# Kernel optimization log

Hardware: AMD Instinct MI355X
Metric: run time of the kernel (lower is better)

Reference implementation:

```python
import jax, jax.numpy as jnp
import numpy as np

B, H, S, DK = 2, 8, 4096, 64


def setup_inputs() -> dict:
    key = jax.random.key(0)
    kq, kk, kv = jax.random.split(key, 3)
    Q = jax.random.normal(kq, (B, H, S, DK), dtype=jnp.float32)
    K = jax.random.normal(kk, (B, H, S, DK), dtype=jnp.float32)
    V = jax.random.normal(kv, (B, H, S, DK), dtype=jnp.float32)
    attn_mask = jnp.zeros((1,), dtype=bool)  # accepted but unused by the module
    return {"Q": Q, "K": K, "V": V, "attn_mask": attn_mask}


def reference(Q, K, V, attn_mask):
    d_k = Q.shape[-1]
    scale = 1.0 / np.sqrt(d_k).astype(np.float32)
    # scores: [b, h, q, k] -- full O(n^2) matrix, as in the original
    scores = jnp.einsum('bhqd,bhkd->bhqk', Q, K) * scale
    attn = jax.nn.softmax(scores, axis=-1)
    context = jnp.einsum('bhqk,bhkd->bhqd', attn, V)
    return (context, attn)
```

## Files before the change

### kernel.cpp

```cpp
#include <hip/hip_runtime.h>
#include <hip/hip_bf16.h>


typedef __bf16 bf16x8 __attribute__((ext_vector_type(8)));
typedef __bf16 bf16x4 __attribute__((ext_vector_type(4)));
typedef float f32x4 __attribute__((ext_vector_type(4)));

#define BH 16
#define SEQ 4096
#define DKD 64
#define PSTRIDE 72
#define LOG2E 1.44269504088896f

__global__ void cvt_bf16_kernel(const float* __restrict__ src,
                                __bf16* __restrict__ dst, int n4, float scale) {
    int i = blockIdx.x * blockDim.x + threadIdx.x;
    if (i < n4) {
        const float4 v = reinterpret_cast<const float4*>(src)[i];
        bf16x4 o;
        o[0] = (__bf16)(v.x * scale); o[1] = (__bf16)(v.y * scale);
        o[2] = (__bf16)(v.z * scale); o[3] = (__bf16)(v.w * scale);
        reinterpret_cast<bf16x4*>(dst)[i] = o;
    }
}

__global__ void transpose_v_kernel(const float* __restrict__ V,
                                   __bf16* __restrict__ Vt) {
    __shared__ __bf16 T[DKD][72];
    const int head = blockIdx.y;
    const int s0 = blockIdx.x * 64;
    const int t = threadIdx.x;
    const float* vp = V + ((size_t)head * SEQ + s0) * DKD;
#pragma unroll
    for (int i = 0; i < 16; ++i) {
        int j = i * 256 + t;
        T[j & 63][j >> 6] = (__bf16)vp[j];
    }
    __syncthreads();
    __bf16* op = Vt + (size_t)head * DKD * SEQ + s0;
#pragma unroll
    for (int i = 0; i < 16; ++i) {
        int j = i * 256 + t;
        op[(size_t)(j >> 6) * SEQ + (j & 63)] = T[j >> 6][j & 63];
    }
}

__global__ __launch_bounds__(256, 4) void attn_kernel(
    const __bf16* __restrict__ Qb, const __bf16* __restrict__ Kb,
    const __bf16* __restrict__ Vt, float* __restrict__ out_ctx,
    float* __restrict__ out_attn) {
    __shared__ __align__(16) __bf16 Pl[2][4][16][PSTRIDE];
    __shared__ float Lsum[4][16];

    const int tid = threadIdx.x;
    const int w = tid >> 6;
    const int lane = tid & 63;
    const int c16 = lane & 15;
    const int g = lane >> 4;
    const int qsub = w & 1;
    const int khalf = w >> 1;

    const int wg = blockIdx.x;
    const int head = ((wg & 7) << 1) | ((wg >> 3) & 1);
    const int qblk = wg >> 4;
    const int qbase = qblk * 32 + qsub * 16;
    const int tile0 = khalf * 32;

    const __bf16* qp = Qb + ((size_t)head * SEQ + qbase + c16) * DKD + g * 8;
    const bf16x8 qf0 = *reinterpret_cast<const bf16x8*>(qp);
    const bf16x8 qf1 = *reinterpret_cast<const bf16x8*>(qp + 32);

    const __bf16* kbase = Kb + (size_t)head * SEQ * DKD;
    const __bf16* vbase = Vt + (size_t)head * DKD * SEQ;
    float* attn_p = out_attn + ((size_t)head * SEQ + qbase) * SEQ;

    float lsum = 0.f;
    for (int t = 0; t < 32; ++t) {
        const int kt = (tile0 + t) * 64;
#pragma unroll
        for (int ct = 0; ct < 4; ++ct) {
            const __bf16* kp = kbase + (size_t)(kt + ct * 16 + c16) * DKD + g * 8;
            bf16x8 kf0 = *reinterpret_cast<const bf16x8*>(kp);
            bf16x8 kf1 = *reinterpret_cast<const bf16x8*>(kp + 32);
            f32x4 a = (f32x4){0.f, 0.f, 0.f, 0.f};
            a = __builtin_amdgcn_mfma_f32_16x16x32_bf16(kf0, qf0, a, 0, 0, 0);
            a = __builtin_amdgcn_mfma_f32_16x16x32_bf16(kf1, qf1, a, 0, 0, 0);
            float e0 = __builtin_amdgcn_exp2f(a[0] * LOG2E);
            float e1 = __builtin_amdgcn_exp2f(a[1] * LOG2E);
            float e2 = __builtin_amdgcn_exp2f(a[2] * LOG2E);
            float e3 = __builtin_amdgcn_exp2f(a[3] * LOG2E);
            lsum += (e0 + e1) + (e2 + e3);
        }
    }
    lsum += __shfl_xor(lsum, 16);
    lsum += __shfl_xor(lsum, 32);
    if (g == 0) Lsum[w][c16] = lsum;
    __syncthreads();
    const float inv_l = __builtin_amdgcn_rcpf(Lsum[w][c16] + Lsum[w ^ 2][c16]);

    f32x4 o[4];
#pragma unroll
    for (int dt = 0; dt < 4; ++dt) o[dt] = (f32x4){0.f, 0.f, 0.f, 0.f};

    auto computeS = [&](int t, __bf16(*Pbuf)[PSTRIDE]) {
        const int kt = (tile0 + t) * 64;
        f32x4 acc[4];
#pragma unroll
        for (int ct = 0; ct < 4; ++ct) {
            acc[ct] = (f32x4){0.f, 0.f, 0.f, 0.f};
            const __bf16* kp = kbase + (size_t)(kt + ct * 16 + c16) * DKD + g * 8;
            bf16x8 kf0 = *reinterpret_cast<const bf16x8*>(kp);
            bf16x8 kf1 = *reinterpret_cast<const bf16x8*>(kp + 32);
            acc[ct] = __builtin_amdgcn_mfma_f32_16x16x32_bf16(kf0, qf0, acc[ct], 0, 0, 0);
            acc[ct] = __builtin_amdgcn_mfma_f32_16x16x32_bf16(kf1, qf1, acc[ct], 0, 0, 0);
        }
#pragma unroll
        for (int ct = 0; ct < 4; ++ct) {
            bf16x4 pb;
#pragma unroll
            for (int r = 0; r < 4; ++r)
                pb[r] = (__bf16)(__builtin_amdgcn_exp2f(acc[ct][r] * LOG2E) * inv_l);
            *reinterpret_cast<bf16x4*>(&Pbuf[c16][ct * 16 + g * 4]) = pb;
        }
    };

    auto pvTile = [&](int t, const __bf16(*Pbuf)[PSTRIDE]) {
        const int kt = (tile0 + t) * 64;
        bf16x8 pb0 = *reinterpret_cast<const bf16x8*>(&Pbuf[c16][g * 8]);
        bf16x8 pb1 = *reinterpret_cast<const bf16x8*>(&Pbuf[c16][g * 8 + 32]);
#pragma unroll
        for (int dt = 0; dt < 4; ++dt) {
            const __bf16* vp = vbase + (size_t)(dt * 16 + c16) * SEQ + kt + g * 8;
            bf16x8 vf0 = *reinterpret_cast<const bf16x8*>(vp);
            bf16x8 vf1 = *reinterpret_cast<const bf16x8*>(vp + 32);
            o[dt] = __builtin_amdgcn_mfma_f32_16x16x32_bf16(vf0, pb0, o[dt], 0, 0, 0);
            o[dt] = __builtin_amdgcn_mfma_f32_16x16x32_bf16(vf1, pb1, o[dt], 0, 0, 0);
        }
    };

    auto storeAttn = [&](int t, const __bf16(*Pbuf)[PSTRIDE]) {
        const int kt = (tile0 + t) * 64;
#pragma unroll
        for (int r4 = 0; r4 < 4; ++r4) {
            const int row = r4 * 4 + g;
            bf16x4 pb = *reinterpret_cast<const bf16x4*>(&Pbuf[row][c16 * 4]);
            f32x4 v;
#pragma unroll
            for (int j = 0; j < 4; ++j) v[j] = (float)pb[j];
            *reinterpret_cast<f32x4*>(attn_p + (size_t)row * SEQ + kt + c16 * 4) = v;
        }
    };

    computeS(0, Pl[0][w]);
    for (int t = 1; t < 31; t += 2) {
        computeS(t, Pl[1][w]);
        pvTile(t - 1, Pl[0][w]);
        storeAttn(t - 1, Pl[0][w]);
        computeS(t + 1, Pl[0][w]);
        pvTile(t, Pl[1][w]);
        storeAttn(t, Pl[1][w]);
    }
    computeS(31, Pl[1][w]);
    pvTile(30, Pl[0][w]);
    storeAttn(30, Pl[0][w]);
    pvTile(31, Pl[1][w]);
    storeAttn(31, Pl[1][w]);

    __syncthreads();
    float* Of = reinterpret_cast<float*>(&Pl[0][0][0][0]);
    float* my = Of + ((size_t)qsub * 16 + c16) * 64;
    if (khalf == 1) {
#pragma unroll
        for (int dt = 0; dt < 4; ++dt)
            *reinterpret_cast<f32x4*>(my + dt * 16 + g * 4) = o[dt];
    }
    __syncthreads();
    if (khalf == 0) {
        float* ctx_p = out_ctx + ((size_t)head * SEQ + qbase) * DKD;
#pragma unroll
        for (int dt = 0; dt < 4; ++dt) {
            f32x4 p = *reinterpret_cast<const f32x4*>(my + dt * 16 + g * 4);
            o[dt] += p;
            *reinterpret_cast<f32x4*>(ctx_p + (size_t)c16 * DKD + dt * 16 + g * 4) = o[dt];
        }
    }
}

extern "C" void kernel_launch(void* const* d_in, const int* in_sizes, int n_in,
                              void* d_out, int out_size, void* d_ws, size_t ws_size,
                              hipStream_t stream) {
    const float* Q = (const float*)d_in[0];
    const float* K = (const float*)d_in[1];
    const float* V = (const float*)d_in[2];
    float* out = (float*)d_out;

    const size_t nElem = (size_t)BH * SEQ * DKD;
    __bf16* Qb = (__bf16*)d_ws;
    __bf16* Kb = Qb + nElem;
    __bf16* Vt = Kb + nElem;

    float* out_ctx = out;
    float* out_attn = out + nElem;

    const int n4 = (int)(nElem / 4);
    cvt_bf16_kernel<<<dim3((n4 + 255) / 256), dim3(256), 0, stream>>>(Q, Qb, n4, 0.125f);
    cvt_bf16_kernel<<<dim3((n4 + 255) / 256), dim3(256), 0, stream>>>(K, Kb, n4, 1.0f);
    transpose_v_kernel<<<dim3(64, BH), dim3(256), 0, stream>>>(V, Vt);
    attn_kernel<<<dim3(BH * SEQ / 32), dim3(256), 0, stream>>>(Qb, Kb, Vt, out_ctx, out_attn);
}
```

Baseline: 765.4 us.

## Split row-sum pass into its own kernel and store fp32 attn directly from registers

The softmax denominator pass moves into a separate lsum kernel that writes the row sums to workspace, and the main kernel reads them back. This frees the attention kernel from the shared-memory sum buffer and its block barrier. The attention probabilities are now written in fp32 straight from the MFMA accumulators instead of being reread from bf16 shared memory. That gives full fp32 precision in attn and removes an LDS round trip. The trade-off is an extra kernel launch and strided 16-byte stores per row, which may coalesce worse than the previous row-contiguous stores.

```diff
diff --git a/kernel.cpp b/kernel.cpp
--- a/kernel.cpp
+++ b/kernel.cpp
@@ -45,11 +45,9 @@
     }
 }
 
-__global__ __launch_bounds__(256, 4) void attn_kernel(
+__global__ __launch_bounds__(256, 4) void lsum_kernel(
     const __bf16* __restrict__ Qb, const __bf16* __restrict__ Kb,
-    const __bf16* __restrict__ Vt, float* __restrict__ out_ctx,
-    float* __restrict__ out_attn) {
-    __shared__ __align__(16) __bf16 Pl[2][4][16][PSTRIDE];
+    float* __restrict__ Lsum_ws) {
     __shared__ float Lsum[4][16];
 
     const int tid = threadIdx.x;
@@ -69,10 +67,7 @@
     const __bf16* qp = Qb + ((size_t)head * SEQ + qbase + c16) * DKD + g * 8;
     const bf16x8 qf0 = *reinterpret_cast<const bf16x8*>(qp);
     const bf16x8 qf1 = *reinterpret_cast<const bf16x8*>(qp + 32);
-
     const __bf16* kbase = Kb + (size_t)head * SEQ * DKD;
-    const __bf16* vbase = Vt + (size_t)head * DKD * SEQ;
-    float* attn_p = out_attn + ((size_t)head * SEQ + qbase) * SEQ;
 
     float lsum = 0.f;
     for (int t = 0; t < 32; ++t) {
@@ -96,7 +91,39 @@
     lsum += __shfl_xor(lsum, 32);
     if (g == 0) Lsum[w][c16] = lsum;
     __syncthreads();
-    const float inv_l = __builtin_amdgcn_rcpf(Lsum[w][c16] + Lsum[w ^ 2][c16]);
+    if (khalf == 0 && g == 0)
+        Lsum_ws[(size_t)head * SEQ + qbase + c16] = Lsum[w][c16] + Lsum[w ^ 2][c16];
+}
+
+__global__ __launch_bounds__(256, 4) void attn_kernel(
+    const __bf16* __restrict__ Qb, const __bf16* __restrict__ Kb,
+    const __bf16* __restrict__ Vt, const float* __restrict__ Lsum_ws,
+    float* __restrict__ out_ctx, float* __restrict__ out_attn) {
+    __shared__ __align__(16) __bf16 Pl[2][4][16][PSTRIDE];
+
+    const int tid = threadIdx.x;
+    const int w = tid >> 6;
+    const int lane = tid & 63;
+    const int c16 = lane & 15;
+    const int g = lane >> 4;
+    const int qsub = w & 1;
+    const int khalf = w >> 1;
+
+    const int wg = blockIdx.x;
+    const int head = ((wg & 7) << 1) | ((wg >> 3) & 1);
+    const int qblk = wg >> 4;
+    const int qbase = qblk * 32 + qsub * 16;
+    const int tile0 = khalf * 32;
+
+    const __bf16* qp = Qb + ((size_t)head * SEQ + qbase + c16) * DKD + g * 8;
+    const bf16x8 qf0 = *reinterpret_cast<const bf16x8*>(qp);
+    const bf16x8 qf1 = *reinterpret_cast<const bf16x8*>(qp + 32);
+
+    const __bf16* kbase = Kb + (size_t)head * SEQ * DKD;
+    const __bf16* vbase = Vt + (size_t)head * DKD * SEQ;
+    float* attn_p = out_attn + ((size_t)head * SEQ + qbase) * SEQ;
+
+    const float inv_l = __builtin_amdgcn_rcpf(Lsum_ws[(size_t)head * SEQ + qbase + c16]);
 
     f32x4 o[4];
 #pragma unroll
@@ -116,10 +143,14 @@
         }
 #pragma unroll
         for (int ct = 0; ct < 4; ++ct) {
+            f32x4 p;
             bf16x4 pb;
 #pragma unroll
-            for (int r = 0; r < 4; ++r)
-                pb[r] = (__bf16)(__builtin_amdgcn_exp2f(acc[ct][r] * LOG2E) * inv_l);
+            for (int r = 0; r < 4; ++r) {
+                p[r] = __builtin_amdgcn_exp2f(acc[ct][r] * LOG2E) * inv_l;
+                pb[r] = (__bf16)p[r];
+            }
+            *reinterpret_cast<f32x4*>(attn_p + (size_t)c16 * SEQ + kt + ct * 16 + g * 4) = p;
             *reinterpret_cast<bf16x4*>(&Pbuf[c16][ct * 16 + g * 4]) = pb;
         }
     };
@@ -138,33 +169,16 @@
         }
     };
 
-    auto storeAttn = [&](int t, const __bf16(*Pbuf)[PSTRIDE]) {
-        const int kt = (tile0 + t) * 64;
-#pragma unroll
-        for (int r4 = 0; r4 < 4; ++r4) {
-            const int row = r4 * 4 + g;
-            bf16x4 pb = *reinterpret_cast<const bf16x4*>(&Pbuf[row][c16 * 4]);
-            f32x4 v;
-#pragma unroll
-            for (int j = 0; j < 4; ++j) v[j] = (float)pb[j];
-            *reinterpret_cast<f32x4*>(attn_p + (size_t)row * SEQ + kt + c16 * 4) = v;
-        }
-    };
-
     computeS(0, Pl[0][w]);
     for (int t = 1; t < 31; t += 2) {
         computeS(t, Pl[1][w]);
         pvTile(t - 1, Pl[0][w]);
-        storeAttn(t - 1, Pl[0][w]);
         computeS(t + 1, Pl[0][w]);
         pvTile(t, Pl[1][w]);
-        storeAttn(t, Pl[1][w]);
     }
     computeS(31, Pl[1][w]);
     pvTile(30, Pl[0][w]);
-    storeAttn(30, Pl[0][w]);
     pvTile(31, Pl[1][w]);
-    storeAttn(31, Pl[1][w]);
 
     __syncthreads();
     float* Of = reinterpret_cast<float*>(&Pl[0][0][0][0]);
@@ -198,6 +212,7 @@
     __bf16* Qb = (__bf16*)d_ws;
     __bf16* Kb = Qb + nElem;
     __bf16* Vt = Kb + nElem;
+    float* Lsum_ws = reinterpret_cast<float*>(Vt + nElem);
 
     float* out_ctx = out;
     float* out_attn = out + nElem;
@@ -206,5 +221,7 @@
     cvt_bf16_kernel<<<dim3((n4 + 255) / 256), dim3(256), 0, stream>>>(Q, Qb, n4, 0.125f);
     cvt_bf16_kernel<<<dim3((n4 + 255) / 256), dim3(256), 0, stream>>>(K, Kb, n4, 1.0f);
     transpose_v_kernel<<<dim3(64, BH), dim3(256), 0, stream>>>(V, Vt);
-    attn_kernel<<<dim3(BH * SEQ / 32), dim3(256), 0, stream>>>(Qb, Kb, Vt, out_ctx, out_attn);
-}
+    lsum_kernel<<<dim3(BH * SEQ / 32), dim3(256), 0, stream>>>(Qb, Kb, Lsum_ws);
+    attn_kernel<<<dim3(BH * SEQ / 32), dim3(256), 0, stream>>>(Qb, Kb, Vt, Lsum_ws,
+                                                               out_ctx, out_attn);
+}
```

New measurement: 811.2 us. 6.0% more time.
